# Kernel optimization log

Hardware: AMD Instinct MI355X
Metric: run time of the kernel (lower is better)

Reference implementation:

```python
import jax, jax.numpy as jnp
import numpy as np
from jax import lax

NUM_CLASSES = 21      # VOC: background (class 0) + 20 fg classes
TOP_K = 200           # max detections kept per (image, class)
CONF_THRESH = 0.01
NMS_THRESH = 0.45
VAR0, VAR1 = 0.1, 0.2 # cfg.VARIANCE
K_PRE = 256           # candidates pre-selected per class before NMS (fixed-shape NMS)


def setup_inputs() -> dict:
    key = jax.random.key(0)
    k1, k2, k3 = jax.random.split(key, 3)
    B, P, C = 32, 8732, NUM_CLASSES
    loc_data = jax.random.normal(k1, (B, P, 4), dtype=jnp.float32)
    conf_data = jax.random.normal(k2, (B, P, C), dtype=jnp.float32)
    u = jax.random.uniform(k3, (P, 4), dtype=jnp.float32)
    # priors in center-offset form: centers in [0,1), w/h in [0.02, 0.32)
    prior_data = jnp.concatenate([u[:, :2], 0.02 + 0.3 * u[:, 2:]], axis=-1)
    return {"loc_data": loc_data, "conf_data": conf_data, "prior_data": prior_data}


def decode(loc, priors):
    # loc, priors: [..., 4]; priors are (cx, cy, w, h)
    centers = priors[..., :2] + loc[..., :2] * VAR0 * priors[..., 2:]
    wh = priors[..., 2:] * jnp.exp(loc[..., 2:] * VAR1)
    xy_min = centers - wh * 0.5
    return jnp.concatenate([xy_min, xy_min + wh], axis=-1)  # (x1,y1,x2,y2)


def pairwise_iou(b):
    # b: [K, 4] corner boxes -> [K, K] IoU
    area = jnp.maximum(b[:, 2] - b[:, 0], 0.0) * jnp.maximum(b[:, 3] - b[:, 1], 0.0)
    lt = jnp.maximum(b[:, None, :2], b[None, :, :2])
    rb = jnp.minimum(b[:, None, 2:], b[None, :, 2:])
    wh = jnp.clip(rb - lt, 0.0)
    inter = wh[..., 0] * wh[..., 1]
    union = area[:, None] + area[None, :] - inter
    return inter / jnp.maximum(union, 1e-9)


def nms_one_class(scores_p, boxes_p4):
    # scores_p: [P], boxes_p4: [P, 4]; fixed-shape NMS -> [TOP_K, 5] (score, x1, y1, x2, y2)
    vals, idx = lax.top_k(scores_p, K_PRE)          # sorted descending
    cand = boxes_p4[idx]                            # [K_PRE, 4]
    valid = vals > CONF_THRESH
    iou = pairwise_iou(cand)                        # [K_PRE, K_PRE]
    ar = jnp.arange(K_PRE)

    def step(keep, i):
        # a kept box suppresses later boxes overlapping it above threshold
        sup = keep[i] & (iou[i] > NMS_THRESH) & (ar > i)
        return keep & (~sup), None

    keep, _ = lax.scan(step, valid, ar)
    kept_scores = jnp.where(keep, vals, 0.0)
    # kept entries are already score-ordered; pull the top TOP_K survivors to the front
    sv, si = lax.top_k(kept_scores, TOP_K)
    out_boxes = jnp.where(sv[:, None] > 0.0, cand[si], 0.0)
    return jnp.concatenate([sv[:, None], out_boxes], axis=-1)  # [TOP_K, 5]


def reference(loc_data, conf_data, prior_data):
    # loc_data: [B, P, 4], conf_data: [B, P, C], prior_data: [P, 4]
    probs = jax.nn.softmax(conf_data, axis=-1)                     # [B, P, C]
    probs_fg = jnp.swapaxes(probs[..., 1:], 1, 2)                  # [B, C-1, P] (skip background)
    boxes = decode(loc_data, prior_data[None, :, :])               # [B, P, 4]
    # vmap over classes, then over batch
    per_class = jax.vmap(nms_one_class, in_axes=(0, None))         # ([C-1,P],[P,4]) -> [C-1,TOP_K,5]
    per_image = jax.vmap(per_class, in_axes=(0, 0))
    return per_image(probs_fg, boxes)                              # [B, C-1, TOP_K, 5]
```

## Files before the change

### kernel.cpp

```cpp
#include <hip/hip_runtime.h>
#include <stdint.h>

typedef unsigned long long ull;
typedef float f4v __attribute__((ext_vector_type(4)));

#define NUM_CLASSES 21
#define NFG 20
#define TOPK 200
#define KPRE 256
#define NTHR 512
#define CONF_TH 0.01f
#define NMS_TH 0.45f
#define VAR0 0.1f
#define VAR1 0.2f
#define NV9 9
#define T16_LO 0x3C23u
#define T16_HI 0x3F81u
#define BSLOT(g) ((g) + ((g) >> 6))

__global__ __launch_bounds__(256) void rownorm16_kernel(
    const float* __restrict__ conf, float2* __restrict__ norm,
    ushort* __restrict__ probs16, int B, int P) {
    __shared__ __align__(16) float buf[256 * NUM_CLASSES];
    __shared__ __align__(16) ushort b16[NFG * 256];
    const int t = threadIdx.x;
    const int nch = (P + 255) >> 8;

    const int id = blockIdx.x;
    int b, chk;
    if ((B & 7) == 0) {
        int r = id & 7, m = id >> 3;
        int q = m / nch;
        b = r + (q << 3);
        chk = m - q * nch;
    } else {
        b = id / nch;
        chk = id - b * nch;
    }
    const int p0 = chk << 8;
    const int cnt = min(256, P - p0);
    const float* src = conf + ((size_t)b * P + p0) * NUM_CLASSES;

    if (cnt == 256) {
        const f4v* s4 = (const f4v*)src;
        f4v* b4 = (f4v*)buf;
#pragma unroll
        for (int k = 0; k < 6; ++k) {
            int i = (k << 8) + t;
            if (i < (256 * NUM_CLASSES) / 4) b4[i] = s4[i];
        }
    } else {
        int n = cnt * NUM_CLASSES;
        for (int i = t; i < n; i += 256) buf[i] = src[i];
    }
    __syncthreads();

    if (t < cnt) {
        const float* row = buf + t * NUM_CLASSES;
        float x[NUM_CLASSES];
        float mx = row[0];
        x[0] = mx;
#pragma unroll
        for (int j = 1; j < NUM_CLASSES; ++j) { x[j] = row[j]; mx = fmaxf(mx, x[j]); }
        float s = 0.f;
#pragma unroll
        for (int j = 0; j < NUM_CLASSES; ++j) { x[j] = expf(x[j] - mx); s += x[j]; }
        ull nv = (ull)__float_as_uint(mx) | ((ull)__float_as_uint(s) << 32);
        __hip_atomic_store((ull*)(norm + (size_t)b * P + p0 + t), nv,
                           __ATOMIC_RELAXED, __HIP_MEMORY_SCOPE_AGENT);
#pragma unroll
        for (int c = 1; c < NUM_CLASSES; ++c) {
            float v = x[c] / s;
            b16[(c - 1) * 256 + t] = (ushort)(__float_as_uint(v) >> 16);
        }
    }
    __syncthreads();

    if (cnt == 256) {
        const uint* s32 = (const uint*)b16;
#pragma unroll
        for (int k = 0; k < 10; ++k) {
            int e = (k << 8) + t;
            int c = e >> 7;
            int q = e & 127;
            uint* dstu = (uint*)(probs16 + ((size_t)b * NFG + c) * P + p0);
            __hip_atomic_store(dstu + q, s32[(c << 7) + q],
                               __ATOMIC_RELAXED, __HIP_MEMORY_SCOPE_AGENT);
        }
    } else {
        for (int e = t; e < NFG * cnt; e += 256) {
            int c = e / cnt;
            int f = e - c * cnt;
            __hip_atomic_store(probs16 + ((size_t)b * NFG + c) * P + p0 + f,
                               b16[c * 256 + f],
                               __ATOMIC_RELAXED, __HIP_MEMORY_SCOPE_AGENT);
        }
    }
}

__global__ __launch_bounds__(NTHR) void nms_topk_kernel(
    const float* __restrict__ conf, const float2* __restrict__ norm,
    const ushort* __restrict__ probs16, const float* __restrict__ loc,
    const float* __restrict__ prior, float* __restrict__ out, int B, int P) {

    __shared__ ull arr[2 * KPRE];
    __shared__ ull arr2[2 * KPRE];
    __shared__ int wsum[2][8];
    __shared__ int s_cnt;
    __shared__ float4 sbox[KPRE + (KPRE >> 6)];
    __shared__ float sarea[KPRE + (KPRE >> 6)];
    __shared__ ull smask[KPRE][5];
    __shared__ ull kept_mask[4];

    const int t = threadIdx.x;
    const int lane = t & 63;
    const int wid = t >> 6;
    const ull lmask_lt = (1ULL << lane) - 1ULL;

    const int g = blockIdx.x;
    int b, c;
    if ((B & 7) == 0) {
        int k = g >> 3;
        b = ((k / NFG) << 3) + (g & 7);
        c = k - (k / NFG) * NFG;
    } else {
        b = g / NFG;
        c = g - (g / NFG) * NFG;
    }
    const int pair = b * NFG + c;
    const int nq = P >> 1;

    unsigned int u2[NV9];
    {
        const uint* sp16 = (const uint*)(probs16 + (size_t)pair * P);
#pragma unroll
        for (int i = 0; i < NV9; ++i) {
            int q = (i << 9) + t;
            u2[i] = (q < nq) ? sp16[q] : 0u;
        }
    }

    {
        unsigned int lo = T16_LO, hi = T16_HI;
        while (hi - lo > 1u) {
            unsigned int mid = lo + ((hi - lo) >> 1);
            int cc = 0;
#pragma unroll
            for (int i = 0; i < NV9; ++i) {
                cc += __popcll(__ballot((u2[i] & 0xFFFFu) >= mid));
                cc += __popcll(__ballot((u2[i] >> 16) >= mid));
            }
            if (cc >= KPRE / 8) lo = mid; else hi = mid;
        }
        if (lane == 0) wsum[0][wid] = (int)lo;
    }
    __syncthreads();
    unsigned int T16;
    {
        int m = wsum[0][0];
#pragma unroll
        for (int w = 1; w < 8; ++w) m = min(m, wsum[0][w]);
        T16 = (unsigned int)m;
    }

    int nval;
    for (int attempt = 0;; ++attempt) {
        if (t == 0) s_cnt = 0;
        __syncthreads();
        int wtot = 0;
#pragma unroll
        for (int i = 0; i < NV9; ++i) {
            wtot += __popcll(__ballot((u2[i] & 0xFFFFu) >= T16));
            wtot += __popcll(__ballot((u2[i] >> 16) >= T16));
        }
        int wbase = 0;
        if (lane == 0) wbase = atomicAdd(&s_cnt, wtot);
        wbase = __shfl(wbase, 0);
        int run = wbase;
#pragma unroll
        for (int i = 0; i < NV9; ++i) {
#pragma unroll
            for (int h = 0; h < 2; ++h) {
                unsigned int bits16 = h ? (u2[i] >> 16) : (u2[i] & 0xFFFFu);
                bool pred = (bits16 >= T16);
                ull bal = __ballot(pred);
                if (pred) {
                    int slot = run + __popcll(bal & lmask_lt);
                    if (slot < 2 * KPRE)
                        arr[slot] = (ull)(unsigned int)((((i << 9) + t) << 1) + h);
                }
                run += __popcll(bal);
            }
        }
        __syncthreads();
        if (s_cnt <= 2 * KPRE || attempt == 1) { nval = min(s_cnt, 2 * KPRE); break; }
        unsigned int lo = T16, hi = T16_HI;
        int it = 0;
        while (hi - lo > 1u) {
            unsigned int mid = lo + ((hi - lo) >> 1);
            int cc = 0;
#pragma unroll
            for (int i = 0; i < NV9; ++i) {
                cc += __popcll(__ballot((u2[i] & 0xFFFFu) >= mid));
                cc += __popcll(__ballot((u2[i] >> 16) >= mid));
            }
            if (lane == 0) wsum[it & 1][wid] = cc;
            __syncthreads();
            int totc = 0;
#pragma unroll
            for (int w = 0; w < 8; ++w) totc += wsum[it & 1][w];
            if (totc >= KPRE) lo = mid; else hi = mid;
            ++it;
        }
        T16 = lo;
    }

    if (t >= nval) arr[t] = (ull)0xFFFFFFFFu;
    __syncthreads();

    const float* cb = conf + (size_t)b * P * NUM_CLASSES + (c + 1);
    const float2* nb = norm + (size_t)b * P;
    ull k0;
    {
        unsigned int pa = (unsigned int)arr[t];
        if (pa < (unsigned int)P) {
            float xa = cb[(size_t)pa * NUM_CLASSES];
            float2 ma = nb[pa];
            float v = expf(xa - ma.x) / ma.y;
            k0 = ((ull)__float_as_uint(v) << 32) | (unsigned int)(~pa);
        } else {
            k0 = 0ULL;
        }
    }
    __syncthreads();

    {
        int lstage = 0;
#pragma unroll
        for (int kk = 2; kk <= 2 * KPRE; kk <<= 1) {
#pragma unroll
            for (int j = kk >> 1; j > 0; j >>= 1) {
                bool amLow = ((t & j) == 0);
                bool d0 = ((t & kk) == 0);
                if (j >= 64) {
                    ull* A = (lstage & 1) ? arr : arr2;
                    ++lstage;
                    A[t] = k0;
                    __syncthreads();
                    ull o0 = A[t ^ j];
                    k0 = (d0 == amLow) ? ((k0 > o0) ? k0 : o0) : ((k0 > o0) ? o0 : k0);
                } else {
                    ull o0 = __shfl_xor(k0, j);
                    k0 = (d0 == amLow) ? ((k0 > o0) ? k0 : o0) : ((k0 > o0) ? o0 : k0);
                }
            }
        }
    }
    const ull key = k0;

    float v = 0.f, x1 = 0.f, y1 = 0.f, x2 = 0.f, y2 = 0.f;
    if (t < KPRE) {
        v = __uint_as_float((unsigned int)(key >> 32));
        int idx = (int)(~(unsigned int)(key & 0xFFFFFFFFu));
        if (idx < 0 || idx >= P) { idx = 0; v = 0.f; }

        const float4 lv = *(const float4*)(loc + ((size_t)b * P + idx) * 4);
        const float4 pv = *(const float4*)(prior + (size_t)idx * 4);
        float cx = pv.x + (lv.x * VAR0) * pv.z;
        float cy = pv.y + (lv.y * VAR0) * pv.w;
        float w = pv.z * expf(lv.z * VAR1);
        float h = pv.w * expf(lv.w * VAR1);
        x1 = cx - w * 0.5f;
        y1 = cy - h * 0.5f;
        x2 = x1 + w;
        y2 = y1 + h;
        float myarea = fmaxf(x2 - x1, 0.f) * fmaxf(y2 - y1, 0.f);
        sbox[BSLOT(t)] = make_float4(x1, y1, x2, y2);
        sarea[BSLOT(t)] = myarea;
    }
    __syncthreads();

#pragma unroll
    for (int rep = 0; rep < 2; ++rep) {
        int pid = t + (rep << 9);
        if (pid < 640) {
            int r, w2;
            if (pid < 64)       { r = pid;                w2 = 0; }
            else if (pid < 192) { int q = pid - 64;  r = 64  + (q >> 1); w2 = q & 1; }
            else if (pid < 384) { int q = pid - 192; int q3 = q / 3; r = 128 + q3; w2 = q - 3 * q3; }
            else                { int q = pid - 384; r = 192 + (q >> 2); w2 = q & 3; }
            float4 rb = sbox[BSLOT(r)];
            float ra = sarea[BSLOT(r)];
            ull mm = 0ULL;
            for (int i = 0; i < 64; ++i) {
                int gg = (w2 << 6) + i;
                float4 gb = sbox[BSLOT(gg)];
                float lx = fmaxf(gb.x, rb.x), ly = fmaxf(gb.y, rb.y);
                float rx = fminf(gb.z, rb.z), ry = fminf(gb.w, rb.w);
                float iw = fmaxf(rx - lx, 0.f), ih = fmaxf(ry - ly, 0.f);
                float inter = iw * ih;
                float uni = sarea[BSLOT(gg)] + ra - inter;
                bool s = (inter / fmaxf(uni, 1e-9f)) > NMS_TH;
                mm |= ((ull)(s ? 1u : 0u)) << i;
            }
            smask[r][w2] = mm;
        }
    }
    __syncthreads();

    ull m0 = 0ULL, m1 = 0ULL, m2 = 0ULL, m3 = 0ULL;
    if (t < KPRE) {
        m0 = smask[t][0];
        m1 = (wid >= 1) ? smask[t][1] : 0ULL;
        m2 = (wid >= 2) ? smask[t][2] : 0ULL;
        m3 = (wid >= 3) ? smask[t][3] : 0ULL;
        if (wid == 0) m0 &= lmask_lt;
        else if (wid == 1) m1 &= lmask_lt;
        else if (wid == 2) m2 &= lmask_lt;
        else m3 &= lmask_lt;
    }

    int alive = (t < KPRE && v > CONF_TH) ? 1 : 0;
    ull mykept = 0ULL;
#pragma unroll
    for (int w2 = 0; w2 < 4; ++w2) {
        if (wid == w2) {
            if (w2 > 0 && (m0 & kept_mask[0])) alive = 0;
            if (w2 > 1 && (m1 & kept_mask[1])) alive = 0;
            if (w2 > 2 && (m2 & kept_mask[2])) alive = 0;
            ull mw = (w2 == 0) ? m0 : (w2 == 1) ? m1 : (w2 == 2) ? m2 : m3;
            ull validb = __ballot(alive != 0);
            ull todo = __ballot((mw & validb) != 0ULL) & validb;
            ull kept = validb & ~todo;
            while (todo) {
                int i = __builtin_ctzll(todo);
                ull row = __shfl(mw, i);
                if ((row & kept) == 0ULL) kept |= (1ULL << i);
                todo &= (todo - 1ULL);
            }
            mykept = kept;
            alive = (int)((kept >> lane) & 1ULL);
            if (lane == 0) kept_mask[w2] = kept;
        }
        __syncthreads();
    }

    int rank = 0;
#pragma unroll
    for (int w2 = 0; w2 < 4; ++w2)
        if (w2 < wid) rank += __popcll(kept_mask[w2]);
    rank += __popcll(mykept & lmask_lt);
    int total = 0;
#pragma unroll
    for (int w2 = 0; w2 < 4; ++w2) total += __popcll(kept_mask[w2]);

    float* orow = out + (size_t)pair * TOPK * 5;
    if (alive && rank < TOPK) {
        float* o = orow + rank * 5;
        o[0] = v; o[1] = x1; o[2] = y1; o[3] = x2; o[4] = y2;
    }
    if (t < TOPK && t >= total) {
        float* o = orow + t * 5;
        o[0] = 0.f; o[1] = 0.f; o[2] = 0.f; o[3] = 0.f; o[4] = 0.f;
    }
}

extern "C" void kernel_launch(void* const* d_in, const int* in_sizes, int n_in,
                              void* d_out, int out_size, void* d_ws, size_t ws_size,
                              hipStream_t stream) {
    const float* loc = (const float*)d_in[0];
    const float* conf = (const float*)d_in[1];
    const float* prior = (const float*)d_in[2];
    float* out = (float*)d_out;

    int P = in_sizes[2] / 4;
    int B = in_sizes[0] / (4 * P);
    int nch = (P + 255) / 256;

    float2* norm = (float2*)d_ws;
    ushort* probs16 = (ushort*)((char*)d_ws + (size_t)B * P * 8);

    rownorm16_kernel<<<dim3(B * nch), 256, 0, stream>>>(conf, norm, probs16, B, P);
    nms_topk_kernel<<<B * NFG, NTHR, 0, stream>>>(conf, norm, probs16, loc, prior, out, B, P);
}
```

Measured before the change: 122.1 us.

## Build NMS suppression masks with wave ballots and division-free IoU test

```diff
diff --git a/kernel.cpp b/kernel.cpp
--- a/kernel.cpp
+++ b/kernel.cpp
@@ -130,13 +130,15 @@
     const int pair = b * NFG + c;
     const int nq = P >> 1;
 
-    unsigned int u2[NV9];
+    unsigned int lo16[NV9], hi16[NV9];
     {
         const uint* sp16 = (const uint*)(probs16 + (size_t)pair * P);
 #pragma unroll
         for (int i = 0; i < NV9; ++i) {
             int q = (i << 9) + t;
-            u2[i] = (q < nq) ? sp16[q] : 0u;
+            unsigned int u = (q < nq) ? sp16[q] : 0u;
+            lo16[i] = u & 0xFFFFu;
+            hi16[i] = u >> 16;
         }
     }
 
@@ -147,8 +149,8 @@
             int cc = 0;
 #pragma unroll
             for (int i = 0; i < NV9; ++i) {
-                cc += __popcll(__ballot((u2[i] & 0xFFFFu) >= mid));
-                cc += __popcll(__ballot((u2[i] >> 16) >= mid));
+                cc += __popcll(__ballot(lo16[i] >= mid));
+                cc += __popcll(__ballot(hi16[i] >= mid));
             }
             if (cc >= KPRE / 8) lo = mid; else hi = mid;
         }
@@ -170,8 +172,8 @@
         int wtot = 0;
 #pragma unroll
         for (int i = 0; i < NV9; ++i) {
-            wtot += __popcll(__ballot((u2[i] & 0xFFFFu) >= T16));
-            wtot += __popcll(__ballot((u2[i] >> 16) >= T16));
+            wtot += __popcll(__ballot(lo16[i] >= T16));
+            wtot += __popcll(__ballot(hi16[i] >= T16));
         }
         int wbase = 0;
         if (lane == 0) wbase = atomicAdd(&s_cnt, wtot);
@@ -181,7 +183,7 @@
         for (int i = 0; i < NV9; ++i) {
 #pragma unroll
             for (int h = 0; h < 2; ++h) {
-                unsigned int bits16 = h ? (u2[i] >> 16) : (u2[i] & 0xFFFFu);
+                unsigned int bits16 = h ? hi16[i] : lo16[i];
                 bool pred = (bits16 >= T16);
                 ull bal = __ballot(pred);
                 if (pred) {
@@ -201,8 +203,8 @@
             int cc = 0;
 #pragma unroll
             for (int i = 0; i < NV9; ++i) {
-                cc += __popcll(__ballot((u2[i] & 0xFFFFu) >= mid));
-                cc += __popcll(__ballot((u2[i] >> 16) >= mid));
+                cc += __popcll(__ballot(lo16[i] >= mid));
+                cc += __popcll(__ballot(hi16[i] >= mid));
             }
             if (lane == 0) wsum[it & 1][wid] = cc;
             __syncthreads();
@@ -280,30 +282,25 @@
     }
     __syncthreads();
 
-#pragma unroll
-    for (int rep = 0; rep < 2; ++rep) {
-        int pid = t + (rep << 9);
-        if (pid < 640) {
-            int r, w2;
-            if (pid < 64)       { r = pid;                w2 = 0; }
-            else if (pid < 192) { int q = pid - 64;  r = 64  + (q >> 1); w2 = q & 1; }
-            else if (pid < 384) { int q = pid - 192; int q3 = q / 3; r = 128 + q3; w2 = q - 3 * q3; }
-            else                { int q = pid - 384; r = 192 + (q >> 2); w2 = q & 3; }
-            float4 rb = sbox[BSLOT(r)];
-            float ra = sarea[BSLOT(r)];
-            ull mm = 0ULL;
-            for (int i = 0; i < 64; ++i) {
-                int gg = (w2 << 6) + i;
-                float4 gb = sbox[BSLOT(gg)];
+    {
+        const double Mth = 30198989.0 / 67108864.0;
+#pragma unroll
+        for (int w2 = 0; w2 < 4; ++w2) {
+            int gg = (w2 << 6) + lane;
+            float4 gb = sbox[BSLOT(gg)];
+            float ga = sarea[BSLOT(gg)];
+            for (int r = (w2 << 6) + wid; r < KPRE; r += 8) {
+                float4 rb = sbox[BSLOT(r)];
+                float ra = sarea[BSLOT(r)];
                 float lx = fmaxf(gb.x, rb.x), ly = fmaxf(gb.y, rb.y);
                 float rx = fminf(gb.z, rb.z), ry = fminf(gb.w, rb.w);
                 float iw = fmaxf(rx - lx, 0.f), ih = fmaxf(ry - ly, 0.f);
                 float inter = iw * ih;
-                float uni = sarea[BSLOT(gg)] + ra - inter;
-                bool s = (inter / fmaxf(uni, 1e-9f)) > NMS_TH;
-                mm |= ((ull)(s ? 1u : 0u)) << i;
-            }
-            smask[r][w2] = mm;
+                float uni = fmaxf(ga + ra - inter, 1e-9f);
+                bool s = ((double)inter > Mth * (double)uni);
+                ull bal = __ballot(s);
+                if (lane == 0) smask[r][w2] = bal;
+            }
         }
     }
     __syncthreads();
```

Measured after the change: 119.6 us. 2.1% less time.
